# Performance work log

Measured on AMD Instinct MI355X. Metric: run time of the kernel, lower is better.

## Reference

```python
import jax, jax.numpy as jnp
import numpy as np

EDGE_DIM = 64
NODE_DIM = 64
HIDDEN_DIM = 256
N_EDGES = 1_000_000
N_NODES = 100_000


def setup_inputs() -> dict:
    key = jax.random.key(0)
    k_e, k_v, k_idx, k_w1, k_b1, k_w2, k_b2 = jax.random.split(key, 7)
    E = jax.random.normal(k_e, (N_EDGES, EDGE_DIM), dtype=jnp.float32)
    V = jax.random.normal(k_v, (N_NODES, NODE_DIM), dtype=jnp.float32)
    edge_index = jax.random.randint(k_idx, (2, N_EDGES), 0, N_NODES, dtype=jnp.int64)
    in_dim = EDGE_DIM + 2 * NODE_DIM  # 192
    # Kaiming-uniform-ish init like torch Linear defaults
    lim1 = 1.0 / np.sqrt(in_dim)
    lim2 = 1.0 / np.sqrt(HIDDEN_DIM)
    W1 = jax.random.uniform(k_w1, (in_dim, HIDDEN_DIM), jnp.float32, -lim1, lim1)
    b1 = jax.random.uniform(k_b1, (HIDDEN_DIM,), jnp.float32, -lim1, lim1)
    W2 = jax.random.uniform(k_w2, (HIDDEN_DIM, HIDDEN_DIM), jnp.float32, -lim2, lim2)
    b2 = jax.random.uniform(k_b2, (HIDDEN_DIM,), jnp.float32, -lim2, lim2)
    return {"E": E, "V": V, "edge_index": edge_index,
            "W1": W1, "b1": b1, "W2": W2, "b2": b2}


def reference(E, V, edge_index, W1, b1, W2, b2):
    src = edge_index[0]
    dst = edge_index[1]
    v_src = V[src]                       # [N_e, F_v] gather
    v_dst = V[dst]                       # [N_e, F_v] gather
    x = jnp.concatenate([E, v_src, v_dst], axis=-1)  # [N_e, F_e + 2*F_v]
    h = jax.nn.relu(x @ W1 + b1)         # [N_e, hidden]
    return h @ W2 + b2                   # [N_e, hidden]
```

## Files before the change

### kernel.cpp

```cpp
#include <hip/hip_runtime.h>
#include <hip/hip_bf16.h>

#define N_EDGES_C 1000000
#define EDGE_DIM_C 64
#define NODE_DIM_C 64
#define IN_DIM_C   192
#define HID_C      256
#define XPAD 200
#define XBUF_SZ 25600
#define HS_OFF  51200
#define HBUF_SZ 32768
#define T_TILES 5

typedef __attribute__((ext_vector_type(8))) short  short8;
typedef __attribute__((ext_vector_type(4))) float  f32x4;

#define BAR_LDS() asm volatile("s_waitcnt lgkmcnt(0)\n\ts_barrier" ::: "memory")

__device__ __forceinline__ unsigned short f2bf(float f) {
    union { float f; unsigned u; } v; v.f = f;
    unsigned u = v.u;
    u += 0x7fffu + ((u >> 16) & 1u);
    return (unsigned short)(u >> 16);
}

__global__ void prep_weights_kernel(const float* __restrict__ W1,
                                    const float* __restrict__ W2,
                                    unsigned short* __restrict__ W1T,
                                    unsigned short* __restrict__ W2T) {
    int tid = blockIdx.x * 256 + threadIdx.x;
    if (tid < IN_DIM_C * HID_C) {
        int n = tid / IN_DIM_C, k = tid - n * IN_DIM_C;
        W1T[tid] = f2bf(W1[k * HID_C + n]);
    } else {
        int t2 = tid - IN_DIM_C * HID_C;
        if (t2 < HID_C * HID_C) {
            int o = t2 / HID_C, k = t2 - o * HID_C;
            W2T[t2] = f2bf(W2[k * HID_C + o]);
        }
    }
}

__global__ __launch_bounds__(512, 2) void edge_mlp_kernel(
    const float* __restrict__ E, const float* __restrict__ V,
    const int* __restrict__ srcI, const int* __restrict__ dstI,
    const unsigned short* __restrict__ W1T, const float* __restrict__ b1,
    const unsigned short* __restrict__ W2T, const float* __restrict__ b2,
    float* __restrict__ out)
{
    __shared__ unsigned char smem[HS_OFF + 2 * HBUF_SZ];
    const int tid = threadIdx.x;
    const int w  = tid >> 6;
    const int l  = tid & 63;
    const int lm = l & 15;
    const int lg = l >> 4;
    const long block0 = (long)blockIdx.x * (64 * T_TILES);

    short8 wA1[6][2];
    short8 wA2[8][2];
#pragma unroll
    for (int kb = 0; kb < 6; ++kb)
#pragma unroll
        for (int nt = 0; nt < 2; ++nt)
            wA1[kb][nt] = *reinterpret_cast<const short8*>(
                W1T + (size_t)(w * 32 + nt * 16 + lm) * IN_DIM_C + kb * 32 + lg * 8);
#pragma unroll
    for (int kb = 0; kb < 8; ++kb)
#pragma unroll
        for (int ot = 0; ot < 2; ++ot)
            wA2[kb][ot] = *reinterpret_cast<const short8*>(
                W2T + (size_t)(w * 32 + ot * 16 + lm) * HID_C + kb * 32 + lg * 8);

    f32x4 fE[2];
    f32x4 fV[4];

    const int kind = (l >> 3) & 1;
    const int rr   = l & 7;
    const int* const ip = kind ? dstI : srcI;

    auto load_idx = [&](long tb) -> int {
        return ip[tb + w * 8 + rr];
    };

    auto issueEV = [&](long tb, int myidx) {
#pragma unroll
        for (int i = 0; i < 2; ++i) {
            int f = i * 64 + l;
            fE[i] = __builtin_nontemporal_load(reinterpret_cast<const f32x4*>(
                E + (size_t)(tb + w * 8 + (f >> 4)) * EDGE_DIM_C + (f & 15) * 4));
        }
#pragma unroll
        for (int i = 0; i < 4; ++i) {
            int kind2 = ((l & 31) < 16) ? 0 : 1;
            int srcl  = kind2 * 8 + i * 2 + (l >> 5);
            int gi = __builtin_amdgcn_ds_bpermute(srcl << 2, myidx);
            fV[i] = *reinterpret_cast<const f32x4*>(
                V + (size_t)gi * NODE_DIM_C + (l & 15) * 4);
        }
    };

    auto write_lds = [&](int buf) {
        unsigned short* Xs = (unsigned short*)(smem + buf * XBUF_SZ);
#pragma unroll
        for (int i = 0; i < 2; ++i) {
            int f = i * 64 + l;
            ushort4 b;
            b.x = f2bf(fE[i][0]); b.y = f2bf(fE[i][1]);
            b.z = f2bf(fE[i][2]); b.w = f2bf(fE[i][3]);
            *reinterpret_cast<ushort4*>(
                &Xs[(w * 8 + (f >> 4)) * XPAD + (f & 15) * 4]) = b;
        }
#pragma unroll
        for (int i = 0; i < 4; ++i) {
            int kind2 = ((l & 31) < 16) ? 0 : 1;
            int rV    = i * 2 + (l >> 5);
            ushort4 b;
            b.x = f2bf(fV[i][0]); b.y = f2bf(fV[i][1]);
            b.z = f2bf(fV[i][2]); b.w = f2bf(fV[i][3]);
            *reinterpret_cast<ushort4*>(
                &Xs[(w * 8 + rV) * XPAD + 64 + kind2 * 64 + (l & 15) * 4]) = b;
        }
    };

    {
        int idx0 = load_idx(block0);
        issueEV(block0, idx0);
        write_lds(0);
    }
    int idxNext = (T_TILES > 1) ? load_idx(block0 + 64) : 0;
    BAR_LDS();

#pragma unroll 1
    for (int t = 0; t < T_TILES; ++t) {
        const long tb = block0 + (long)t * 64;
        const int xb = t & 1;

        if (t + 1 < T_TILES) issueEV(tb + 64, idxNext);
        if (t + 2 < T_TILES) idxNext = load_idx(tb + 128);

        const unsigned short* Xs = (const unsigned short*)(smem + xb * XBUF_SZ);
        f32x4 acc[2][4];
#pragma unroll
        for (int a = 0; a < 2; ++a)
#pragma unroll
            for (int b = 0; b < 4; ++b)
                acc[a][b] = (f32x4){0.f, 0.f, 0.f, 0.f};

        __builtin_amdgcn_s_setprio(1);
#pragma unroll
        for (int kb = 0; kb < 6; ++kb) {
            short8 bx[4];
#pragma unroll
            for (int mt = 0; mt < 4; ++mt)
                bx[mt] = *reinterpret_cast<const short8*>(
                    &Xs[(mt * 16 + lm) * XPAD + kb * 32 + lg * 8]);
#pragma unroll
            for (int nt = 0; nt < 2; ++nt)
#pragma unroll
                for (int mt = 0; mt < 4; ++mt)
                    acc[nt][mt] = __builtin_amdgcn_mfma_f32_16x16x32_bf16(
                        wA1[kb][nt], bx[mt], acc[nt][mt], 0, 0, 0);
        }
        __builtin_amdgcn_s_setprio(0);

        unsigned char* Hb = smem + HS_OFF + xb * HBUF_SZ;
#pragma unroll
        for (int nt = 0; nt < 2; ++nt) {
            int n0 = w * 32 + nt * 16 + lg * 4;
            float4 bv = *reinterpret_cast<const float4*>(b1 + n0);
#pragma unroll
            for (int mt = 0; mt < 4; ++mt) {
                f32x4 a = acc[nt][mt];
                ushort4 hb;
                hb.x = f2bf(fmaxf(a[0] + bv.x, 0.f));
                hb.y = f2bf(fmaxf(a[1] + bv.y, 0.f));
                hb.z = f2bf(fmaxf(a[2] + bv.z, 0.f));
                hb.w = f2bf(fmaxf(a[3] + bv.w, 0.f));
                int m = mt * 16 + lm;
                int addr = m * 512 + ((n0 * 2) ^ (lm << 4));
                *reinterpret_cast<ushort4*>(Hb + addr) = hb;
            }
        }

        if (t + 1 < T_TILES) write_lds(xb ^ 1);

        BAR_LDS();

#pragma unroll
        for (int a = 0; a < 2; ++a)
#pragma unroll
            for (int b = 0; b < 4; ++b)
                acc[a][b] = (f32x4){0.f, 0.f, 0.f, 0.f};

        __builtin_amdgcn_s_setprio(1);
#pragma unroll
        for (int kb = 0; kb < 8; ++kb) {
            short8 bh[4];
#pragma unroll
            for (int mt = 0; mt < 4; ++mt) {
                int m = mt * 16 + lm;
                int addr = m * 512 + (((kb * 32 + lg * 8) * 2) ^ (lm << 4));
                bh[mt] = *reinterpret_cast<const short8*>(Hb + addr);
            }
#pragma unroll
            for (int ot = 0; ot < 2; ++ot)
#pragma unroll
                for (int mt = 0; mt < 4; ++mt)
                    acc[ot][mt] = __builtin_amdgcn_mfma_f32_16x16x32_bf16(
                        wA2[kb][ot], bh[mt], acc[ot][mt], 0, 0, 0);
        }
        __builtin_amdgcn_s_setprio(0);

#pragma unroll
        for (int ot = 0; ot < 2; ++ot) {
            int o0 = w * 32 + ot * 16 + lg * 4;
            float4 bv = *reinterpret_cast<const float4*>(b2 + o0);
#pragma unroll
            for (int mt = 0; mt < 4; ++mt) {
                f32x4 a = acc[ot][mt];
                f32x4 r;
                r[0] = a[0] + bv.x;
                r[1] = a[1] + bv.y;
                r[2] = a[2] + bv.z;
                r[3] = a[3] + bv.w;
                __builtin_nontemporal_store(r, reinterpret_cast<f32x4*>(
                    out + (size_t)(tb + mt * 16 + lm) * HID_C + o0));
            }
        }
    }
}

extern "C" void kernel_launch(void* const* d_in, const int* in_sizes, int n_in,
                              void* d_out, int out_size, void* d_ws, size_t ws_size,
                              hipStream_t stream) {
    const float* E  = (const float*)d_in[0];
    const float* V  = (const float*)d_in[1];
    const int*   ei = (const int*)d_in[2];
    const float* W1 = (const float*)d_in[3];
    const float* b1 = (const float*)d_in[4];
    const float* W2 = (const float*)d_in[5];
    const float* b2 = (const float*)d_in[6];
    float* out = (float*)d_out;

    unsigned short* W1T = (unsigned short*)d_ws;
    unsigned short* W2T = W1T + IN_DIM_C * HID_C;

    const int prep_total = IN_DIM_C * HID_C + HID_C * HID_C;
    prep_weights_kernel<<<(prep_total + 255) / 256, 256, 0, stream>>>(W1, W2, W1T, W2T);

    const int nblocks = N_EDGES_C / (64 * T_TILES);
    edge_mlp_kernel<<<nblocks, 512, 0, stream>>>(
        E, V, ei, ei + N_EDGES_C, W1T, b1, W2T, b2, out);
}
```

Before: 510.0 us.

## Double block to 1024 threads with 16 waves each computing one 16-column slice

Blocks go from 512 to 1024 threads, so each of 16 waves owns a single 16-wide output column tile instead of two. Gather work is redistributed so each thread loads one E row-chunk and one src and one dst V chunk. Bias loads are hoisted out of the tile loop, and the s_setprio hints are removed. Per-wave register use and per-wave work are halved to raise latency hiding. In exchange, every wave re-reads the shared X and H tiles from LDS, doubling LDS read traffic per tile, and the launch bounds of 1024 threads with 4 blocks per CU are likely unattainable given the shared-memory footprint.

New measurement: 578.8 us. 13.5% more time.

```diff
diff --git a/kernel.cpp b/kernel.cpp
--- a/kernel.cpp
+++ b/kernel.cpp
@@ -41,7 +41,7 @@
     }
 }
 
-__global__ __launch_bounds__(512, 2) void edge_mlp_kernel(
+__global__ __launch_bounds__(1024, 4) void edge_mlp_kernel(
     const float* __restrict__ E, const float* __restrict__ V,
     const int* __restrict__ srcI, const int* __restrict__ dstI,
     const unsigned short* __restrict__ W1T, const float* __restrict__ b1,
@@ -50,84 +50,57 @@
 {
     __shared__ unsigned char smem[HS_OFF + 2 * HBUF_SZ];
     const int tid = threadIdx.x;
-    const int w  = tid >> 6;
-    const int l  = tid & 63;
-    const int lm = l & 15;
-    const int lg = l >> 4;
+    const int w   = tid >> 6;
+    const int l   = tid & 63;
+    const int lm  = l & 15;
+    const int lg  = l >> 4;
+    const int r16 = tid >> 4;
+    const int c16 = tid & 15;
     const long block0 = (long)blockIdx.x * (64 * T_TILES);
 
-    short8 wA1[6][2];
-    short8 wA2[8][2];
+    short8 wA1[6];
+    short8 wA2[8];
 #pragma unroll
     for (int kb = 0; kb < 6; ++kb)
-#pragma unroll
-        for (int nt = 0; nt < 2; ++nt)
-            wA1[kb][nt] = *reinterpret_cast<const short8*>(
-                W1T + (size_t)(w * 32 + nt * 16 + lm) * IN_DIM_C + kb * 32 + lg * 8);
+        wA1[kb] = *reinterpret_cast<const short8*>(
+            W1T + (size_t)(w * 16 + lm) * IN_DIM_C + kb * 32 + lg * 8);
 #pragma unroll
     for (int kb = 0; kb < 8; ++kb)
-#pragma unroll
-        for (int ot = 0; ot < 2; ++ot)
-            wA2[kb][ot] = *reinterpret_cast<const short8*>(
-                W2T + (size_t)(w * 32 + ot * 16 + lm) * HID_C + kb * 32 + lg * 8);
-
-    f32x4 fE[2];
-    f32x4 fV[4];
-
-    const int kind = (l >> 3) & 1;
-    const int rr   = l & 7;
-    const int* const ip = kind ? dstI : srcI;
-
-    auto load_idx = [&](long tb) -> int {
-        return ip[tb + w * 8 + rr];
-    };
-
-    auto issueEV = [&](long tb, int myidx) {
-#pragma unroll
-        for (int i = 0; i < 2; ++i) {
-            int f = i * 64 + l;
-            fE[i] = __builtin_nontemporal_load(reinterpret_cast<const f32x4*>(
-                E + (size_t)(tb + w * 8 + (f >> 4)) * EDGE_DIM_C + (f & 15) * 4));
-        }
-#pragma unroll
-        for (int i = 0; i < 4; ++i) {
-            int kind2 = ((l & 31) < 16) ? 0 : 1;
-            int srcl  = kind2 * 8 + i * 2 + (l >> 5);
-            int gi = __builtin_amdgcn_ds_bpermute(srcl << 2, myidx);
-            fV[i] = *reinterpret_cast<const f32x4*>(
-                V + (size_t)gi * NODE_DIM_C + (l & 15) * 4);
-        }
+        wA2[kb] = *reinterpret_cast<const short8*>(
+            W2T + (size_t)(w * 16 + lm) * HID_C + kb * 32 + lg * 8);
+
+    const int n0 = w * 16 + lg * 4;
+    const f32x4 b1v = *reinterpret_cast<const f32x4*>(b1 + n0);
+    const f32x4 b2v = *reinterpret_cast<const f32x4*>(b2 + n0);
+
+    f32x4 fE, fV0, fV1;
+
+    auto issueEV = [&](long tb, int gs, int gd) {
+        fE = __builtin_nontemporal_load(reinterpret_cast<const f32x4*>(
+            E + (size_t)(tb + r16) * EDGE_DIM_C + c16 * 4));
+        fV0 = *reinterpret_cast<const f32x4*>(V + (size_t)gs * NODE_DIM_C + c16 * 4);
+        fV1 = *reinterpret_cast<const f32x4*>(V + (size_t)gd * NODE_DIM_C + c16 * 4);
     };
 
     auto write_lds = [&](int buf) {
         unsigned short* Xs = (unsigned short*)(smem + buf * XBUF_SZ);
-#pragma unroll
-        for (int i = 0; i < 2; ++i) {
-            int f = i * 64 + l;
-            ushort4 b;
-            b.x = f2bf(fE[i][0]); b.y = f2bf(fE[i][1]);
-            b.z = f2bf(fE[i][2]); b.w = f2bf(fE[i][3]);
-            *reinterpret_cast<ushort4*>(
-                &Xs[(w * 8 + (f >> 4)) * XPAD + (f & 15) * 4]) = b;
-        }
-#pragma unroll
-        for (int i = 0; i < 4; ++i) {
-            int kind2 = ((l & 31) < 16) ? 0 : 1;
-            int rV    = i * 2 + (l >> 5);
-            ushort4 b;
-            b.x = f2bf(fV[i][0]); b.y = f2bf(fV[i][1]);
-            b.z = f2bf(fV[i][2]); b.w = f2bf(fV[i][3]);
-            *reinterpret_cast<ushort4*>(
-                &Xs[(w * 8 + rV) * XPAD + 64 + kind2 * 64 + (l & 15) * 4]) = b;
-        }
+        ushort4 a, b, c;
+        a.x = f2bf(fE[0]);  a.y = f2bf(fE[1]);  a.z = f2bf(fE[2]);  a.w = f2bf(fE[3]);
+        b.x = f2bf(fV0[0]); b.y = f2bf(fV0[1]); b.z = f2bf(fV0[2]); b.w = f2bf(fV0[3]);
+        c.x = f2bf(fV1[0]); c.y = f2bf(fV1[1]); c.z = f2bf(fV1[2]); c.w = f2bf(fV1[3]);
+        *reinterpret_cast<ushort4*>(&Xs[r16 * XPAD + c16 * 4])       = a;
+        *reinterpret_cast<ushort4*>(&Xs[r16 * XPAD + 64 + c16 * 4])  = b;
+        *reinterpret_cast<ushort4*>(&Xs[r16 * XPAD + 128 + c16 * 4]) = c;
     };
 
     {
-        int idx0 = load_idx(block0);
-        issueEV(block0, idx0);
+        int gs0 = srcI[block0 + r16];
+        int gd0 = dstI[block0 + r16];
+        issueEV(block0, gs0, gd0);
         write_lds(0);
     }
-    int idxNext = (T_TILES > 1) ? load_idx(block0 + 64) : 0;
+    int gsN = 0, gdN = 0;
+    if (T_TILES > 1) { gsN = srcI[block0 + 64 + r16]; gdN = dstI[block0 + 64 + r16]; }
     BAR_LDS();
 
 #pragma unroll 1
@@ -135,18 +108,17 @@
         const long tb = block0 + (long)t * 64;
         const int xb = t & 1;
 
-        if (t + 1 < T_TILES) issueEV(tb + 64, idxNext);
-        if (t + 2 < T_TILES) idxNext = load_idx(tb + 128);
+        if (t + 1 < T_TILES) issueEV(tb + 64, gsN, gdN);
+        if (t + 2 < T_TILES) {
+            gsN = srcI[tb + 128 + r16];
+            gdN = dstI[tb + 128 + r16];
+        }
 
         const unsigned short* Xs = (const unsigned short*)(smem + xb * XBUF_SZ);
-        f32x4 acc[2][4];
-#pragma unroll
-        for (int a = 0; a < 2; ++a)
-#pragma unroll
-            for (int b = 0; b < 4; ++b)
-                acc[a][b] = (f32x4){0.f, 0.f, 0.f, 0.f};
-
-        __builtin_amdgcn_s_setprio(1);
+        f32x4 acc[4];
+#pragma unroll
+        for (int m = 0; m < 4; ++m) acc[m] = (f32x4){0.f, 0.f, 0.f, 0.f};
+
 #pragma unroll
         for (int kb = 0; kb < 6; ++kb) {
             short8 bx[4];
@@ -155,44 +127,33 @@
                 bx[mt] = *reinterpret_cast<const short8*>(
                     &Xs[(mt * 16 + lm) * XPAD + kb * 32 + lg * 8]);
 #pragma unroll
-            for (int nt = 0; nt < 2; ++nt)
-#pragma unroll
-                for (int mt = 0; mt < 4; ++mt)
-                    acc[nt][mt] = __builtin_amdgcn_mfma_f32_16x16x32_bf16(
-                        wA1[kb][nt], bx[mt], acc[nt][mt], 0, 0, 0);
-        }
-        __builtin_amdgcn_s_setprio(0);
+            for (int mt = 0; mt < 4; ++mt)
+                acc[mt] = __builtin_amdgcn_mfma_f32_16x16x32_bf16(
+                    wA1[kb], bx[mt], acc[mt], 0, 0, 0);
+        }
 
         unsigned char* Hb = smem + HS_OFF + xb * HBUF_SZ;
 #pragma unroll
-        for (int nt = 0; nt < 2; ++nt) {
-            int n0 = w * 32 + nt * 16 + lg * 4;
-            float4 bv = *reinterpret_cast<const float4*>(b1 + n0);
-#pragma unroll
-            for (int mt = 0; mt < 4; ++mt) {
-                f32x4 a = acc[nt][mt];
-                ushort4 hb;
-                hb.x = f2bf(fmaxf(a[0] + bv.x, 0.f));
-                hb.y = f2bf(fmaxf(a[1] + bv.y, 0.f));
-                hb.z = f2bf(fmaxf(a[2] + bv.z, 0.f));
-                hb.w = f2bf(fmaxf(a[3] + bv.w, 0.f));
-                int m = mt * 16 + lm;
-                int addr = m * 512 + ((n0 * 2) ^ (lm << 4));
-                *reinterpret_cast<ushort4*>(Hb + addr) = hb;
-            }
+        for (int mt = 0; mt < 4; ++mt) {
+            f32x4 a = acc[mt];
+            ushort4 hb;
+            hb.x = f2bf(fmaxf(a[0] + b1v[0], 0.f));
+            hb.y = f2bf(fmaxf(a[1] + b1v[1], 0.f));
+            hb.z = f2bf(fmaxf(a[2] + b1v[2], 0.f));
+            hb.w = f2bf(fmaxf(a[3] + b1v[3], 0.f));
+            int m = mt * 16 + lm;
+            int addr = m * 512 + ((n0 * 2) ^ (lm << 4));
+            *reinterpret_cast<ushort4*>(Hb + addr) = hb;
         }
 
         if (t + 1 < T_TILES) write_lds(xb ^ 1);
 
         BAR_LDS();
 
-#pragma unroll
-        for (int a = 0; a < 2; ++a)
-#pragma unroll
-            for (int b = 0; b < 4; ++b)
-                acc[a][b] = (f32x4){0.f, 0.f, 0.f, 0.f};
-
-        __builtin_amdgcn_s_setprio(1);
+        f32x4 acc2[4];
+#pragma unroll
+        for (int m = 0; m < 4; ++m) acc2[m] = (f32x4){0.f, 0.f, 0.f, 0.f};
+
 #pragma unroll
         for (int kb = 0; kb < 8; ++kb) {
             short8 bh[4];
@@ -203,29 +164,21 @@
                 bh[mt] = *reinterpret_cast<const short8*>(Hb + addr);
             }
 #pragma unroll
-            for (int ot = 0; ot < 2; ++ot)
-#pragma unroll
-                for (int mt = 0; mt < 4; ++mt)
-                    acc[ot][mt] = __builtin_amdgcn_mfma_f32_16x16x32_bf16(
-                        wA2[kb][ot], bh[mt], acc[ot][mt], 0, 0, 0);
-        }
-        __builtin_amdgcn_s_setprio(0);
-
-#pragma unroll
-        for (int ot = 0; ot < 2; ++ot) {
-            int o0 = w * 32 + ot * 16 + lg * 4;
-            float4 bv = *reinterpret_cast<const float4*>(b2 + o0);
-#pragma unroll
-            for (int mt = 0; mt < 4; ++mt) {
-                f32x4 a = acc[ot][mt];
-                f32x4 r;
-                r[0] = a[0] + bv.x;
-                r[1] = a[1] + bv.y;
-                r[2] = a[2] + bv.z;
-                r[3] = a[3] + bv.w;
-                __builtin_nontemporal_store(r, reinterpret_cast<f32x4*>(
-                    out + (size_t)(tb + mt * 16 + lm) * HID_C + o0));
-            }
+            for (int mt = 0; mt < 4; ++mt)
+                acc2[mt] = __builtin_amdgcn_mfma_f32_16x16x32_bf16(
+                    wA2[kb], bh[mt], acc2[mt], 0, 0, 0);
+        }
+
+#pragma unroll
+        for (int mt = 0; mt < 4; ++mt) {
+            f32x4 a = acc2[mt];
+            f32x4 r;
+            r[0] = a[0] + b2v[0];
+            r[1] = a[1] + b2v[1];
+            r[2] = a[2] + b2v[2];
+            r[3] = a[3] + b2v[3];
+            __builtin_nontemporal_store(r, reinterpret_cast<f32x4*>(
+                out + (size_t)(tb + mt * 16 + lm) * HID_C + n0));
         }
     }
 }
@@ -249,6 +202,6 @@
     prep_weights_kernel<<<(prep_total + 255) / 256, 256, 0, stream>>>(W1, W2, W1T, W2T);
 
     const int nblocks = N_EDGES_C / (64 * T_TILES);
-    edge_mlp_kernel<<<nblocks, 512, 0, stream>>>(
+    edge_mlp_kernel<<<nblocks, 1024, 0, stream>>>(
         E, V, ei, ei + N_EDGES_C, W1T, b1, W2T, b2, out);
 }
```

## Phase GEMM loops with block barriers to synchronize LDS reads and MFMA bursts

Applied to the files above, without the earlier changes.

Splits both GEMM k-loops into phases of two k-blocks. Each phase first loads all of its LDS fragments, then hits a block barrier and an lgkmcnt wait, then runs a raised-priority burst of MFMAs, then hits another barrier. The aim is to keep all waves in step, so LDS reads and matrix-core work line up across the workgroup, like ping-pong style scheduling. The cost is many extra block-wide barriers per tile, which can stall waves and hide less of the global load latency.

After: 575.3 us. +12.8%, slower.

```diff
diff --git a/kernel.cpp b/kernel.cpp
--- a/kernel.cpp
+++ b/kernel.cpp
@@ -16,6 +16,9 @@
 typedef __attribute__((ext_vector_type(4))) float  f32x4;
 
 #define BAR_LDS() asm volatile("s_waitcnt lgkmcnt(0)\n\ts_barrier" ::: "memory")
+#define BAR()     asm volatile("s_barrier" ::: "memory")
+#define LGKM0()   do { asm volatile("s_waitcnt lgkmcnt(0)" ::: "memory"); \
+                       __builtin_amdgcn_sched_barrier(0); } while (0)
 
 __device__ __forceinline__ unsigned short f2bf(float f) {
     union { float f; unsigned u; } v; v.f = f;
@@ -100,7 +103,7 @@
     };
 
     auto write_lds = [&](int buf) {
-        unsigned short* Xs = (unsigned short*)(smem + buf * XBUF_SZ);
+        unsigned short* Xw = (unsigned short*)(smem + buf * XBUF_SZ);
 #pragma unroll
         for (int i = 0; i < 2; ++i) {
             int f = i * 64 + l;
@@ -108,7 +111,7 @@
             b.x = f2bf(fE[i][0]); b.y = f2bf(fE[i][1]);
             b.z = f2bf(fE[i][2]); b.w = f2bf(fE[i][3]);
             *reinterpret_cast<ushort4*>(
-                &Xs[(w * 8 + (f >> 4)) * XPAD + (f & 15) * 4]) = b;
+                &Xw[(w * 8 + (f >> 4)) * XPAD + (f & 15) * 4]) = b;
         }
 #pragma unroll
         for (int i = 0; i < 4; ++i) {
@@ -118,7 +121,7 @@
             b.x = f2bf(fV[i][0]); b.y = f2bf(fV[i][1]);
             b.z = f2bf(fV[i][2]); b.w = f2bf(fV[i][3]);
             *reinterpret_cast<ushort4*>(
-                &Xs[(w * 8 + rV) * XPAD + 64 + kind2 * 64 + (l & 15) * 4]) = b;
+                &Xw[(w * 8 + rV) * XPAD + 64 + kind2 * 64 + (l & 15) * 4]) = b;
         }
     };
 
@@ -139,6 +142,8 @@
         if (t + 2 < T_TILES) idxNext = load_idx(tb + 128);
 
         const unsigned short* Xs = (const unsigned short*)(smem + xb * XBUF_SZ);
+        unsigned char* Hb = smem + HS_OFF + xb * HBUF_SZ;
+
         f32x4 acc[2][4];
 #pragma unroll
         for (int a = 0; a < 2; ++a)
@@ -146,24 +151,31 @@
             for (int b = 0; b < 4; ++b)
                 acc[a][b] = (f32x4){0.f, 0.f, 0.f, 0.f};
 
-        __builtin_amdgcn_s_setprio(1);
-#pragma unroll
-        for (int kb = 0; kb < 6; ++kb) {
-            short8 bx[4];
-#pragma unroll
-            for (int mt = 0; mt < 4; ++mt)
-                bx[mt] = *reinterpret_cast<const short8*>(
-                    &Xs[(mt * 16 + lm) * XPAD + kb * 32 + lg * 8]);
-#pragma unroll
-            for (int nt = 0; nt < 2; ++nt)
+#pragma unroll
+        for (int ph = 0; ph < 3; ++ph) {
+            const int kb0 = ph * 2;
+            short8 bx[2][4];
+#pragma unroll
+            for (int k = 0; k < 2; ++k)
 #pragma unroll
                 for (int mt = 0; mt < 4; ++mt)
-                    acc[nt][mt] = __builtin_amdgcn_mfma_f32_16x16x32_bf16(
-                        wA1[kb][nt], bx[mt], acc[nt][mt], 0, 0, 0);
-        }
-        __builtin_amdgcn_s_setprio(0);
-
-        unsigned char* Hb = smem + HS_OFF + xb * HBUF_SZ;
+                    bx[k][mt] = *reinterpret_cast<const short8*>(
+                        &Xs[(mt * 16 + lm) * XPAD + (kb0 + k) * 32 + lg * 8]);
+            BAR();
+            LGKM0();
+            __builtin_amdgcn_s_setprio(1);
+#pragma unroll
+            for (int k = 0; k < 2; ++k)
+#pragma unroll
+                for (int nt = 0; nt < 2; ++nt)
+#pragma unroll
+                    for (int mt = 0; mt < 4; ++mt)
+                        acc[nt][mt] = __builtin_amdgcn_mfma_f32_16x16x32_bf16(
+                            wA1[kb0 + k][nt], bx[k][mt], acc[nt][mt], 0, 0, 0);
+            __builtin_amdgcn_s_setprio(0);
+            BAR();
+        }
+
 #pragma unroll
         for (int nt = 0; nt < 2; ++nt) {
             int n0 = w * 32 + nt * 16 + lg * 4;
@@ -181,9 +193,7 @@
                 *reinterpret_cast<ushort4*>(Hb + addr) = hb;
             }
         }
-
         if (t + 1 < T_TILES) write_lds(xb ^ 1);
-
         BAR_LDS();
 
 #pragma unroll
@@ -192,24 +202,32 @@
             for (int b = 0; b < 4; ++b)
                 acc[a][b] = (f32x4){0.f, 0.f, 0.f, 0.f};
 
-        __builtin_amdgcn_s_setprio(1);
-#pragma unroll
-        for (int kb = 0; kb < 8; ++kb) {
-            short8 bh[4];
-#pragma unroll
-            for (int mt = 0; mt < 4; ++mt) {
-                int m = mt * 16 + lm;
-                int addr = m * 512 + (((kb * 32 + lg * 8) * 2) ^ (lm << 4));
-                bh[mt] = *reinterpret_cast<const short8*>(Hb + addr);
-            }
-#pragma unroll
-            for (int ot = 0; ot < 2; ++ot)
-#pragma unroll
-                for (int mt = 0; mt < 4; ++mt)
-                    acc[ot][mt] = __builtin_amdgcn_mfma_f32_16x16x32_bf16(
-                        wA2[kb][ot], bh[mt], acc[ot][mt], 0, 0, 0);
-        }
-        __builtin_amdgcn_s_setprio(0);
+#pragma unroll
+        for (int ph = 0; ph < 4; ++ph) {
+            const int kb0 = ph * 2;
+            short8 bh[2][4];
+#pragma unroll
+            for (int k = 0; k < 2; ++k)
+#pragma unroll
+                for (int mt = 0; mt < 4; ++mt) {
+                    int m = mt * 16 + lm;
+                    int addr = m * 512 + ((((kb0 + k) * 32 + lg * 8) * 2) ^ (lm << 4));
+                    bh[k][mt] = *reinterpret_cast<const short8*>(Hb + addr);
+                }
+            BAR();
+            LGKM0();
+            __builtin_amdgcn_s_setprio(1);
+#pragma unroll
+            for (int k = 0; k < 2; ++k)
+#pragma unroll
+                for (int ot = 0; ot < 2; ++ot)
+#pragma unroll
+                    for (int mt = 0; mt < 4; ++mt)
+                        acc[ot][mt] = __builtin_amdgcn_mfma_f32_16x16x32_bf16(
+                            wA2[kb0 + k][ot], bh[k][mt], acc[ot][mt], 0, 0, 0);
+            __builtin_amdgcn_s_setprio(0);
+            BAR();
+        }
 
 #pragma unroll
         for (int ot = 0; ot < 2; ++ot) {
```
